# Kernel tuning notes

Hardware: AMD Instinct MI355X
Metric: run time of the kernel (lower is better)

## Reference

```python
import jax, jax.numpy as jnp
import numpy as np

K_TOP = 16
TEMP = 1.0
EPS = 1e-9

def setup_inputs() -> dict:
    key = jax.random.key(0)
    k1, k2, k3 = jax.random.split(key, 3)
    B, H, N, D = 4, 8, 2048, 64
    q = jax.random.normal(k1, (B, H, N, D), dtype=jnp.float32)
    k = jax.random.normal(k2, (B, H, N, D), dtype=jnp.float32)
    u = jax.random.uniform(k3, (B, N, N), dtype=jnp.float32)
    return {"q": q, "k": k, "u": u}

def reference(q, k, u):
    # q, k: [B, H, N, D]; u: uniform noise [B, N, N]
    d_head = q.shape[-1]
    scale = 1.0 / jnp.sqrt(jnp.asarray(d_head, dtype=q.dtype))
    # [B, H, N, N] scores, then mean over heads -> [B, N, N]
    attn_scores = jnp.einsum('bhnd,bhmd->bhnm', q, k) * scale
    logits = attn_scores.mean(axis=1)
    gumbel = -jnp.log(-jnp.log(u + EPS) + EPS)
    probs = jax.nn.softmax((logits + gumbel) / TEMP, axis=-1)
    topk_vals = jax.lax.top_k(probs, K_TOP)[0]          # [B, N, K]
    thresh = topk_vals.min(axis=-1, keepdims=True)      # [B, N, 1]
    sparse_mask = (probs >= thresh).astype(probs.dtype)
    return sparse_mask[:, None, :, :]                   # [B, 1, N, N]
```

## Files before the change

### kernel.cpp

```cpp
#include <hip/hip_runtime.h>
#include <math.h>

#define BB 4
#define HH 8
#define NN 2048
#define DD 64
#define KTOP 16
#define CUT_MARGIN 1e-3f

typedef _Float16 half_t;
typedef __attribute__((ext_vector_type(8))) _Float16 half8;
typedef __attribute__((ext_vector_type(4))) float floatx4;

__device__ __forceinline__ void gl_lds16(const half_t* g, half_t* l) {
    __builtin_amdgcn_global_load_lds(
        (const __attribute__((address_space(1))) void*)g,
        (__attribute__((address_space(3))) void*)l, 16, 0, 0);
}

__global__ __launch_bounds__(256) void split_plain(const float* __restrict__ q,
                                                   const float* __restrict__ kk,
                                                   half_t* __restrict__ qhi,
                                                   half_t* __restrict__ qlo,
                                                   half_t* __restrict__ khi,
                                                   half_t* __restrict__ klo) {
    const int uidx = blockIdx.x * 256 + threadIdx.x;
    const size_t src = (size_t)uidx * 8;

    float a[8], b[8];
    *(float4*)&a[0] = *(const float4*)(q + src);
    *(float4*)&a[4] = *(const float4*)(q + src + 4);
    *(float4*)&b[0] = *(const float4*)(kk + src);
    *(float4*)&b[4] = *(const float4*)(kk + src + 4);
    half8 qh, ql, kh, kl;
#pragma unroll
    for (int e = 0; e < 8; ++e) {
        half_t hq = (half_t)a[e];
        half_t hk = (half_t)b[e];
        qh[e] = hq; ql[e] = (half_t)((a[e] - (float)hq) * 2048.0f);
        kh[e] = hk; kl[e] = (half_t)((b[e] - (float)hk) * 2048.0f);
    }
    *(half8*)(qhi + src) = qh;
    *(half8*)(qlo + src) = ql;
    *(half8*)(khi + src) = kh;
    *(half8*)(klo + src) = kl;
}

__global__ __launch_bounds__(256, 2) void gemm_f16x3(const half_t* __restrict__ qhi,
                                                     const half_t* __restrict__ qlo,
                                                     const half_t* __restrict__ khi,
                                                     const half_t* __restrict__ klo,
                                                     float* __restrict__ L) {
    const int b  = blockIdx.z;
    const int i0 = blockIdx.y * 128;
    const int j0 = blockIdx.x * 128;
    const int tid  = threadIdx.x;
    const int wave = __builtin_amdgcn_readfirstlane(tid >> 6);
    const int lane = tid & 63;
    const int wr = wave >> 1, wc = wave & 1;
    const int lm = lane & 15, quad = lane >> 4;

    __shared__ __align__(16) half_t Ah[2][4096];
    __shared__ __align__(16) half_t Al[2][4096];
    __shared__ __align__(16) half_t Bh[2][4096];
    __shared__ __align__(16) half_t Bl[2][4096];

    const int r_base = ((lane >> 5) << 3) + (lane & 7);
    const int t_l    = (lane >> 3) & 3;

    const half_t* gmat;
    half_t* lmat;
    int rowoff;
    if      (wave == 0) { gmat = qhi; lmat = &Ah[0][0]; rowoff = i0; }
    else if (wave == 1) { gmat = qlo; lmat = &Al[0][0]; rowoff = i0; }
    else if (wave == 2) { gmat = khi; lmat = &Bh[0][0]; rowoff = j0; }
    else                { gmat = klo; lmat = &Bl[0][0]; rowoff = j0; }
    const half_t* glane = gmat + ((size_t)b * HH * NN + rowoff + r_base) * DD + t_l * 8;

#define STAGE(s, bufidx)                                                      \
    {                                                                         \
        const half_t* gs = glane + (size_t)((s) >> 1) * (NN * DD) + ((s)&1) * 32; \
        half_t* ls = lmat + (bufidx)*4096;                                    \
        _Pragma("unroll") for (int i = 0; i < 8; ++i)                         \
            gl_lds16(gs + i * 1024, ls + i * 512);                            \
    }

    floatx4 acc1[4][4], acc2[4][4];
#pragma unroll
    for (int tr = 0; tr < 4; ++tr)
#pragma unroll
        for (int tc = 0; tc < 4; ++tc) {
            acc1[tr][tc] = (floatx4)0.0f;
            acc2[tr][tc] = (floatx4)0.0f;
        }

#define COMPUTE(bufidx)                                                       \
    {                                                                         \
        half8 ah[4], al[4], bh[4], bl[4];                                     \
        _Pragma("unroll") for (int t = 0; t < 4; ++t) {                       \
            const int am = wr * 64 + t * 16 + lm;                             \
            const int bm = wc * 64 + t * 16 + lm;                             \
            const int ai = ((am >> 3) << 8) + (quad << 6) + ((am & 7) << 3);  \
            const int bi = ((bm >> 3) << 8) + (quad << 6) + ((bm & 7) << 3);  \
            ah[t] = *(const half8*)&Ah[bufidx][ai];                           \
            al[t] = *(const half8*)&Al[bufidx][ai];                           \
            bh[t] = *(const half8*)&Bh[bufidx][bi];                           \
            bl[t] = *(const half8*)&Bl[bufidx][bi];                           \
        }                                                                     \
        __builtin_amdgcn_s_setprio(1);                                        \
        _Pragma("unroll") for (int tr = 0; tr < 4; ++tr)                      \
            _Pragma("unroll") for (int tc = 0; tc < 4; ++tc) {                \
                acc1[tr][tc] = __builtin_amdgcn_mfma_f32_16x16x32_f16(        \
                    ah[tr], bh[tc], acc1[tr][tc], 0, 0, 0);                   \
                acc2[tr][tc] = __builtin_amdgcn_mfma_f32_16x16x32_f16(        \
                    ah[tr], bl[tc], acc2[tr][tc], 0, 0, 0);                   \
                acc2[tr][tc] = __builtin_amdgcn_mfma_f32_16x16x32_f16(        \
                    al[tr], bh[tc], acc2[tr][tc], 0, 0, 0);                   \
            }                                                                 \
        __builtin_amdgcn_s_setprio(0);                                        \
    }

    STAGE(0, 0);
    __syncthreads();
#pragma unroll
    for (int ss = 0; ss < 7; ++ss) {
        STAGE(2 * ss + 1, 1);
        COMPUTE(0);
        __syncthreads();
        STAGE(2 * ss + 2, 0);
        COMPUTE(1);
        __syncthreads();
    }
    STAGE(15, 1);
    COMPUTE(0);
    __syncthreads();
    COMPUTE(1);

#undef STAGE
#undef COMPUTE

    const float s1 = 0.015625f;
    const float s2 = 0.015625f / 2048.0f;
#pragma unroll
    for (int tr = 0; tr < 4; ++tr)
#pragma unroll
        for (int r = 0; r < 4; ++r) {
            const int grow = i0 + wr * 64 + tr * 16 + quad * 4 + r;
            float* Lp = L + ((size_t)b * NN + grow) * NN + j0 + wc * 64 + lm;
#pragma unroll
            for (int tc = 0; tc < 4; ++tc)
                Lp[tc * 16] = acc1[tr][tc][r] * s1 + acc2[tr][tc][r] * s2;
        }
}

__device__ __forceinline__ unsigned long long flip64(double x) {
    unsigned long long v = (unsigned long long)__double_as_longlong(x);
    return v ^ ((0ULL - (v >> 63)) | 0x8000000000000000ULL);
}
__device__ __forceinline__ double unflip64(unsigned long long k) {
    unsigned long long v = (k >> 63) ? (k ^ 0x8000000000000000ULL) : ~k;
    return __longlong_as_double((long long)v);
}

__global__ __launch_bounds__(64) void topk_mask(float* __restrict__ LM,
                                                const float* __restrict__ u) {
    const int row  = blockIdx.x;
    const int lane = threadIdx.x;
    float* lrow = LM + (size_t)row * NN;
    const float* urow = u + (size_t)row * NN;

    __shared__ int s_idx[64];

    float z[32];
    unsigned hard = 0;
    float4 lb = *(const float4*)(lrow + lane * 4);
    float4 ub = *(const float4*)(urow + lane * 4);
#pragma unroll
    for (int e = 0; e < 8; ++e) {
        float4 lnx, unx;
        if (e < 7) {
            lnx = *(const float4*)(lrow + (e + 1) * 256 + lane * 4);
            unx = *(const float4*)(urow + (e + 1) * 256 + lane * 4);
        }
        const float* ls = (const float*)&lb;
        const float* us = (const float*)&ub;
#pragma unroll
        for (int s = 0; s < 4; ++s) {
            float w = -__logf(us[s] + 1e-9f);
            z[e * 4 + s] = ls[s] - __logf(w + 1e-9f);
            hard |= (us[s] > 0.999f ? 1u : 0u) << (e * 4 + s);
        }
        lb = lnx; ub = unx;
    }

    float v = z[0];
#pragma unroll
    for (int r = 1; r < 32; ++r) v = fmaxf(v, z[r]);
#pragma unroll
    for (int kS = 2; kS <= 64; kS <<= 1) {
#pragma unroll
        for (int j = kS >> 1; j > 0; j >>= 1) {
            float o = __shfl_xor(v, j, 64);
            bool asc = ((lane & kS) == 0);
            bool lower = ((lane & j) == 0);
            float mn = fminf(v, o), mx = fmaxf(v, o);
            v = (asc == lower) ? mn : mx;
        }
    }
    const float cut = __shfl(v, 48, 64) - CUT_MARGIN;

    int c = 0;
#pragma unroll
    for (int r = 0; r < 32; ++r) {
        bool p = (z[r] >= cut);
        unsigned long long m = __ballot(p);
        if (p) {
            int slot = c + __popcll(m & ((1ULL << lane) - 1ULL));
            if (slot < 64) s_idx[slot] = (r >> 2) * 256 + lane * 4 + (r & 3);
        }
        c += __popcll(m);
    }
    if (c > 64) c = 64;

    unsigned long long key = 0xFFFFFFFFFFFFFFFFULL;
    if (lane < c) {
        int idx = s_idx[lane];
        double uu = (double)urow[idx] + 1e-9;
        double w  = -log(uu);
        double g  = -log(w + 1e-9);
        key = flip64((double)lrow[idx] + g);
    }
#pragma unroll
    for (int kS = 2; kS <= 64; kS <<= 1) {
#pragma unroll
        for (int j = kS >> 1; j > 0; j >>= 1) {
            unsigned long long o = __shfl_xor(key, j, 64);
            bool asc = ((lane & kS) == 0);
            bool lower = ((lane & j) == 0);
            unsigned long long mn = (key < o) ? key : o;
            unsigned long long mx = (key < o) ? o : key;
            key = (asc == lower) ? mn : mx;
        }
    }
    const double thresh = unflip64(__shfl(key, c - KTOP, 64));

    const float t_hi = (float)thresh + 3e-4f;
    const float t_lo = (float)thresh - 3e-4f;
    unsigned bm = hard;
#pragma unroll
    for (int r = 0; r < 32; ++r)
        bm |= ((z[r] <= t_hi && z[r] >= t_lo) ? 1u : 0u) << r;
    while (bm) {
        int t = __builtin_ctz(bm);
        bm &= bm - 1;
        const int idx = (t >> 2) * 256 + lane * 4 + (t & 3);
        double uu = (double)urow[idx] + 1e-9;
        double w  = -log(uu);
        double g  = -log(w + 1e-9);
        double z64 = (double)lrow[idx] + g;
        z[t] = (z64 >= thresh) ? 1.0e30f : -1.0e30f;
    }

#pragma unroll
    for (int e = 0; e < 8; ++e) {
        float o[4];
#pragma unroll
        for (int s = 0; s < 4; ++s)
            o[s] = (z[e * 4 + s] > t_hi) ? 1.0f : 0.0f;
        *(float4*)(lrow + e * 256 + lane * 4) = *(float4*)o;
    }
}

extern "C" void kernel_launch(void* const* d_in, const int* in_sizes, int n_in,
                              void* d_out, int out_size, void* d_ws, size_t ws_size,
                              hipStream_t stream) {
    const float* q = (const float*)d_in[0];
    const float* k = (const float*)d_in[1];
    const float* u = (const float*)d_in[2];
    float* out = (float*)d_out;
    const size_t NQ = (size_t)BB * HH * NN * DD;
    half_t* qhi = (half_t*)d_ws;
    half_t* qlo = qhi + NQ;
    half_t* khi = qlo + NQ;
    half_t* klo = khi + NQ;

    split_plain<<<(int)(NQ / 8 / 256), 256, 0, stream>>>(q, k, qhi, qlo, khi, klo);

    dim3 grid1(NN / 128, NN / 128, BB);
    gemm_f16x3<<<grid1, 256, 0, stream>>>(qhi, qlo, khi, klo, out);

    topk_mask<<<BB * NN, 64, 0, stream>>>(out, u);
}
```

Before: 233.8 us.

## Pre-block split halves by K-chunk and deepen GEMM load pipeline

The split kernel now writes the fp16 hi/lo halves in a K-blocked layout of 32-element chunks per (batch·head, half) plane. Each GEMM stage then loads one contiguous 128x32 slab with simple strided addresses, and LDS fragments are read row-major. The GEMM main loop is restructured to keep two stages in flight. It loads fragments to registers, waits on lgkmcnt, and issues the next global-to-LDS stage into the same buffer before running the MFMAs, using explicit vmcnt waits and barriers. The aim is to overlap global loads with compute and simplify addressing. The risk is LDS bank conflicts from the plain row-major layout, and the hand-written waitcnt scheme must be correct.

```diff
diff --git a/kernel.cpp b/kernel.cpp
--- a/kernel.cpp
+++ b/kernel.cpp
@@ -18,14 +18,19 @@
         (__attribute__((address_space(3))) void*)l, 16, 0, 0);
 }
 
-__global__ __launch_bounds__(256) void split_plain(const float* __restrict__ q,
-                                                   const float* __restrict__ kk,
-                                                   half_t* __restrict__ qhi,
-                                                   half_t* __restrict__ qlo,
-                                                   half_t* __restrict__ khi,
-                                                   half_t* __restrict__ klo) {
+__global__ __launch_bounds__(256) void split_kblock(const float* __restrict__ q,
+                                                    const float* __restrict__ kk,
+                                                    half_t* __restrict__ qhi,
+                                                    half_t* __restrict__ qlo,
+                                                    half_t* __restrict__ khi,
+                                                    half_t* __restrict__ klo) {
     const int uidx = blockIdx.x * 256 + threadIdx.x;
     const size_t src = (size_t)uidx * 8;
+    const int R  = uidx >> 3;
+    const int kg = uidx & 7;
+    const int bh = R >> 11;
+    const int n  = R & 2047;
+    const size_t dst = (((size_t)(bh * 2 + (kg >> 2)) << 11) + n) * 32 + (kg & 3) * 8;
 
     float a[8], b[8];
     *(float4*)&a[0] = *(const float4*)(q + src);
@@ -40,10 +45,10 @@
         qh[e] = hq; ql[e] = (half_t)((a[e] - (float)hq) * 2048.0f);
         kh[e] = hk; kl[e] = (half_t)((b[e] - (float)hk) * 2048.0f);
     }
-    *(half8*)(qhi + src) = qh;
-    *(half8*)(qlo + src) = ql;
-    *(half8*)(khi + src) = kh;
-    *(half8*)(klo + src) = kl;
+    *(half8*)(qhi + dst) = qh;
+    *(half8*)(qlo + dst) = ql;
+    *(half8*)(khi + dst) = kh;
+    *(half8*)(klo + dst) = kl;
 }
 
 __global__ __launch_bounds__(256, 2) void gemm_f16x3(const half_t* __restrict__ qhi,
@@ -65,9 +70,6 @@
     __shared__ __align__(16) half_t Bh[2][4096];
     __shared__ __align__(16) half_t Bl[2][4096];
 
-    const int r_base = ((lane >> 5) << 3) + (lane & 7);
-    const int t_l    = (lane >> 3) & 3;
-
     const half_t* gmat;
     half_t* lmat;
     int rowoff;
@@ -75,69 +77,94 @@
     else if (wave == 1) { gmat = qlo; lmat = &Al[0][0]; rowoff = i0; }
     else if (wave == 2) { gmat = khi; lmat = &Bh[0][0]; rowoff = j0; }
     else                { gmat = klo; lmat = &Bl[0][0]; rowoff = j0; }
-    const half_t* glane = gmat + ((size_t)b * HH * NN + rowoff + r_base) * DD + t_l * 8;
-
-#define STAGE(s, bufidx)                                                      \
+    const half_t* glane0 = gmat + (((size_t)(b * HH) * 2) * NN + rowoff) * 32 + lane * 8;
+
+#define STAGE(sv, bufv)                                                       \
     {                                                                         \
-        const half_t* gs = glane + (size_t)((s) >> 1) * (NN * DD) + ((s)&1) * 32; \
-        half_t* ls = lmat + (bufidx)*4096;                                    \
+        const half_t* gs = glane0 + (size_t)(sv) * (NN * 32);                 \
+        half_t* ls = lmat + (bufv) * 4096;                                    \
         _Pragma("unroll") for (int i = 0; i < 8; ++i)                         \
-            gl_lds16(gs + i * 1024, ls + i * 512);                            \
-    }
-
-    floatx4 acc1[4][4], acc2[4][4];
-#pragma unroll
-    for (int tr = 0; tr < 4; ++tr)
-#pragma unroll
-        for (int tc = 0; tc < 4; ++tc) {
-            acc1[tr][tc] = (floatx4)0.0f;
-            acc2[tr][tc] = (floatx4)0.0f;
-        }
-
-#define COMPUTE(bufidx)                                                       \
+            gl_lds16(gs + i * 512, ls + i * 512);                             \
+    }
+
+#define LOADFRAG(bufv)                                                       \
+    _Pragma("unroll") for (int t = 0; t < 4; ++t) {                          \
+        const int am = wr * 64 + t * 16 + lm;                                \
+        const int bm = wc * 64 + t * 16 + lm;                                \
+        fah[t] = *(const half8*)&Ah[bufv][am * 32 + quad * 8];               \
+        fal[t] = *(const half8*)&Al[bufv][am * 32 + quad * 8];               \
+        fbh[t] = *(const half8*)&Bh[bufv][bm * 32 + quad * 8];               \
+        fbl[t] = *(const half8*)&Bl[bufv][bm * 32 + quad * 8];               \
+    }
+
+#define MFMAS                                                                 \
     {                                                                         \
-        half8 ah[4], al[4], bh[4], bl[4];                                     \
-        _Pragma("unroll") for (int t = 0; t < 4; ++t) {                       \
-            const int am = wr * 64 + t * 16 + lm;                             \
-            const int bm = wc * 64 + t * 16 + lm;                             \
-            const int ai = ((am >> 3) << 8) + (quad << 6) + ((am & 7) << 3);  \
-            const int bi = ((bm >> 3) << 8) + (quad << 6) + ((bm & 7) << 3);  \
-            ah[t] = *(const half8*)&Ah[bufidx][ai];                           \
-            al[t] = *(const half8*)&Al[bufidx][ai];                           \
-            bh[t] = *(const half8*)&Bh[bufidx][bi];                           \
-            bl[t] = *(const half8*)&Bl[bufidx][bi];                           \
-        }                                                                     \
         __builtin_amdgcn_s_setprio(1);                                        \
         _Pragma("unroll") for (int tr = 0; tr < 4; ++tr)                      \
             _Pragma("unroll") for (int tc = 0; tc < 4; ++tc) {                \
                 acc1[tr][tc] = __builtin_amdgcn_mfma_f32_16x16x32_f16(        \
-                    ah[tr], bh[tc], acc1[tr][tc], 0, 0, 0);                   \
+                    fah[tr], fbh[tc], acc1[tr][tc], 0, 0, 0);                 \
                 acc2[tr][tc] = __builtin_amdgcn_mfma_f32_16x16x32_f16(        \
-                    ah[tr], bl[tc], acc2[tr][tc], 0, 0, 0);                   \
+                    fah[tr], fbl[tc], acc2[tr][tc], 0, 0, 0);                 \
                 acc2[tr][tc] = __builtin_amdgcn_mfma_f32_16x16x32_f16(        \
-                    al[tr], bh[tc], acc2[tr][tc], 0, 0, 0);                   \
+                    fal[tr], fbh[tc], acc2[tr][tc], 0, 0, 0);                 \
             }                                                                 \
         __builtin_amdgcn_s_setprio(0);                                        \
     }
 
+#define WAITL0 { asm volatile("s_waitcnt lgkmcnt(0)" ::: "memory");           \
+                 __builtin_amdgcn_sched_barrier(0); }
+#define WAITV8 { asm volatile("s_waitcnt vmcnt(8)" ::: "memory");             \
+                 __builtin_amdgcn_sched_barrier(0); }
+#define WAITV0 { asm volatile("s_waitcnt vmcnt(0)" ::: "memory");             \
+                 __builtin_amdgcn_sched_barrier(0); }
+#define BAR    { __builtin_amdgcn_s_barrier();                                \
+                 __builtin_amdgcn_sched_barrier(0); }
+
+    floatx4 acc1[4][4], acc2[4][4];
+#pragma unroll
+    for (int tr = 0; tr < 4; ++tr)
+#pragma unroll
+        for (int tc = 0; tc < 4; ++tc) {
+            acc1[tr][tc] = (floatx4)0.0f;
+            acc2[tr][tc] = (floatx4)0.0f;
+        }
+
+    half8 fah[4], fal[4], fbh[4], fbl[4];
+
     STAGE(0, 0);
-    __syncthreads();
-#pragma unroll
-    for (int ss = 0; ss < 7; ++ss) {
-        STAGE(2 * ss + 1, 1);
-        COMPUTE(0);
-        __syncthreads();
-        STAGE(2 * ss + 2, 0);
-        COMPUTE(1);
-        __syncthreads();
-    }
-    STAGE(15, 1);
-    COMPUTE(0);
-    __syncthreads();
-    COMPUTE(1);
+    STAGE(1, 1);
+    WAITV8;
+    BAR;
+
+#pragma unroll 2
+    for (int s = 0; s < 14; ++s) {
+        const int cur = s & 1;
+        LOADFRAG(cur);
+        WAITL0;
+        BAR;
+        STAGE(s + 2, cur);
+        MFMAS;
+        WAITV8;
+        BAR;
+    }
+    LOADFRAG(0);
+    WAITL0;
+    BAR;
+    MFMAS;
+    WAITV0;
+    BAR;
+    LOADFRAG(1);
+    WAITL0;
+    MFMAS;
 
 #undef STAGE
-#undef COMPUTE
+#undef LOADFRAG
+#undef MFMAS
+#undef WAITL0
+#undef WAITV8
+#undef WAITV0
+#undef BAR
 
     const float s1 = 0.015625f;
     const float s2 = 0.015625f / 2048.0f;
@@ -284,7 +311,7 @@
     half_t* khi = qlo + NQ;
     half_t* klo = khi + NQ;
 
-    split_plain<<<(int)(NQ / 8 / 256), 256, 0, stream>>>(q, k, qhi, qlo, khi, klo);
+    split_kblock<<<(int)(NQ / 8 / 256), 256, 0, stream>>>(q, k, qhi, qlo, khi, klo);
 
     dim3 grid1(NN / 128, NN / 128, BB);
     gemm_f16x3<<<grid1, 256, 0, stream>>>(qhi, qlo, khi, klo, out);
```

New measurement: 221.6 us. -5.2%, faster.
